# Kernel tuning notes

Hardware: AMD Instinct MI355X
Metric: run time of the kernel (lower is better)

The kernel has to match this reference:

```python
import jax, jax.numpy as jnp
import numpy as np

# Dims: C cells, L gene tokens, E embed, H mlp hidden, M factors, K topk
C, L, E, H, M, K = 16, 8192, 512, 256, 128, 30
TAU = 1.0        # gumbel-softmax temperature
SOFTNESS = 0.01  # soft-mask sharpness
TEMP = 1.0       # logits temperature
EPS = 1e-20


def setup_inputs() -> dict:
    key = jax.random.key(0)
    ks = jax.random.split(key, 7)
    x = jax.random.normal(ks[0], (C, L, E), dtype=jnp.float32)
    key_padding_mask = jax.random.randint(ks[1], (C, L), 0, 2) > 0  # True = valid
    uniform_noise = jax.random.uniform(ks[2], (C, L - 1, M), dtype=jnp.float32)
    W1 = jax.random.normal(ks[3], (E, H), dtype=jnp.float32) * (1.0 / np.sqrt(E))
    b1 = jnp.zeros((H,), dtype=jnp.float32)
    W2 = jax.random.normal(ks[4], (H, M), dtype=jnp.float32) * (1.0 / np.sqrt(H))
    b2 = jnp.zeros((M,), dtype=jnp.float32)
    return {"x": x, "key_padding_mask": key_padding_mask,
            "uniform_noise": uniform_noise,
            "W1": W1, "b1": b1, "W2": W2, "b2": b2}


def reference(x, key_padding_mask, uniform_noise, W1, b1, W2, b2):
    # default gene_subset: drop token 0, keep the rest  -> S = L-1
    xs = x[:, 1:, :]                          # (C, S, E)
    kpm = key_padding_mask[:, 1:]             # (C, S)

    # 2-layer MLP router (dropout p=0 -> identity)
    h = jax.nn.relu(jnp.einsum('cse,eh->csh', xs, W1) + b1)   # (C, S, H)
    logits = (jnp.einsum('csh,hm->csm', h, W2) + b2) / TEMP    # (C, S, M)

    # GumbelTopK, training path: gumbel-softmax then smooth top-k mask
    gumbel = -jnp.log(-jnp.log(uniform_noise + EPS) + EPS)
    perturbed = (logits + gumbel) / TAU
    probs = jax.nn.softmax(perturbed, axis=-1)                 # (C, S, M)
    topk_vals, _ = jax.lax.top_k(probs, K)                     # (C, S, K)
    threshold = topk_vals[..., -1:]                            # (C, S, 1)
    smooth_mask = jax.nn.sigmoid((probs - threshold) / SOFTNESS)
    out = probs * smooth_mask

    # faithful to the source: mask = ~key_padding_mask; probs *= mask
    out = out * (~kpm)[..., None].astype(out.dtype)
    return out, kpm
```

## Files before the change

### kernel.cpp

```cpp
#include <hip/hip_runtime.h>
#include <hip/hip_bf16.h>

#define CC 16
#define LL 8192
#define SS 8191
#define EE 512
#define HH 256
#define MM 128
#define TOPK 30
#define TOT (CC * SS)

typedef __attribute__((ext_vector_type(8))) short short8;
typedef __attribute__((ext_vector_type(4))) float f32x4;
typedef __attribute__((ext_vector_type(4))) unsigned int u32x4;

static __device__ __forceinline__ unsigned short f2bf(float f) {
    unsigned u = __builtin_bit_cast(unsigned, f);
    u += 0x7FFFu + ((u >> 16) & 1u);
    return (unsigned short)(u >> 16);
}

static __device__ __forceinline__ unsigned pk2(float lo, float hi) {
    __hip_bfloat162 t = __float22bfloat162_rn(float2{lo, hi});
    unsigned u;
    __builtin_memcpy(&u, &t, 4);
    return u;
}

static __device__ __forceinline__ short8 cvt8(const float4 a, const float4 b) {
    u32x4 uv;
    uv[0] = pk2(a.x, a.y);
    uv[1] = pk2(a.z, a.w);
    uv[2] = pk2(b.x, b.y);
    uv[3] = pk2(b.z, b.w);
    return __builtin_bit_cast(short8, uv);
}

template<int CTRL>
static __device__ __forceinline__ float dppf(float v) {
    return __builtin_bit_cast(float,
        __builtin_amdgcn_update_dpp(0, __builtin_bit_cast(int, v), CTRL, 0xF, 0xF, false));
}
template<int CTRL>
static __device__ __forceinline__ int dppi(int v) {
    return __builtin_amdgcn_update_dpp(0, v, CTRL, 0xF, 0xF, false);
}
static __device__ __forceinline__ float sum16f(float v) {
    v += dppf<0x121>(v); v += dppf<0x122>(v); v += dppf<0x124>(v); v += dppf<0x128>(v);
    return v;
}
static __device__ __forceinline__ float max16f(float v) {
    v = fmaxf(v, dppf<0x121>(v)); v = fmaxf(v, dppf<0x122>(v));
    v = fmaxf(v, dppf<0x124>(v)); v = fmaxf(v, dppf<0x128>(v));
    return v;
}
static __device__ __forceinline__ unsigned sum16u(unsigned v) {
    v += (unsigned)dppi<0x121>((int)v); v += (unsigned)dppi<0x122>((int)v);
    v += (unsigned)dppi<0x124>((int)v); v += (unsigned)dppi<0x128>((int)v);
    return v;
}

static __device__ __forceinline__ void bar_lgkm() {
    asm volatile("s_waitcnt lgkmcnt(0)" ::: "memory");
    __builtin_amdgcn_sched_barrier(0);
    __builtin_amdgcn_s_barrier();
    __builtin_amdgcn_sched_barrier(0);
}

__global__ void prep_weights(const float* __restrict__ W1, const float* __restrict__ W2,
                             unsigned short* __restrict__ W1T, unsigned short* __restrict__ W2T)
{
    const int b = blockIdx.x, tid = threadIdx.x;
    if (b < 64) {
        const int e0 = b * 8, h = tid;
        short8 sv;
#pragma unroll
        for (int j = 0; j < 8; ++j)
            sv[j] = (short)f2bf(W1[(size_t)(e0 + j) * HH + h]);
        *(short8*)(void*)(W1T + (size_t)h * EE + e0) = sv;
    } else {
        const int h0 = (b - 64) * 16;
        if (tid < MM) {
            const int m = tid;
            short8 s0v, s1v;
#pragma unroll
            for (int j = 0; j < 8; ++j) {
                s0v[j] = (short)f2bf(W2[(size_t)(h0 + j) * MM + m]);
                s1v[j] = (short)f2bf(W2[(size_t)(h0 + 8 + j) * MM + m]);
            }
            *(short8*)(void*)(W2T + (size_t)m * HH + h0) = s0v;
            *(short8*)(void*)(W2T + (size_t)m * HH + h0 + 8) = s1v;
        }
    }
}

__global__ __launch_bounds__(512, 4)
void gene_gemm_kernel(const float* __restrict__ x,
                      const unsigned short* __restrict__ W1T,
                      const float* __restrict__ b1,
                      const unsigned short* __restrict__ W2T,
                      float* __restrict__ logits)
{
    __shared__ __align__(16) unsigned char lds[65536];

    const int tid = threadIdx.x;
    const int c   = blockIdx.y;
    const int s0  = blockIdx.x * 128;

    const int w    = tid >> 6;
    const int lane = tid & 63;
    const int lr   = lane & 15;
    const int kq   = lane >> 4;
    const int wr   = w >> 2;
    const int wc   = w & 3;
    const int cw   = wc * 64;

    const int srow = tid >> 2;
    const int sk4  = tid & 3;
    const int rsc  = min(s0 + srow, SS - 1) - s0;
    const float* xrow = x + ((size_t)c * LL + s0 + 1 + rsc) * EE + sk4 * 16;
    const int swz = (srow & 7) << 4;
    unsigned char* wb = lds + srow * 128;

    float4 xr0, xr1, xr2, xr3;
#define LOADX(ck) do { const float* p_ = xrow + (ck) * 64;                   \
    xr0 = *(const float4*)p_;       xr1 = *(const float4*)(p_ + 4);          \
    xr2 = *(const float4*)(p_ + 8); xr3 = *(const float4*)(p_ + 12); } while (0)

    f32x4 acc[4][4];
#pragma unroll
    for (int r = 0; r < 4; ++r)
#pragma unroll
        for (int n = 0; n < 4; ++n) acc[r][n] = (f32x4)0.0f;

    LOADX(0);

#pragma unroll
    for (int ck = 0; ck < 8; ++ck) {
        const int bo = (ck & 1) << 14;
        *(short8*)(void*)(wb + bo + (((sk4 * 2 + 0) * 16) ^ swz)) = cvt8(xr0, xr1);
        *(short8*)(void*)(wb + bo + (((sk4 * 2 + 1) * 16) ^ swz)) = cvt8(xr2, xr3);
        if (ck < 7) LOADX(ck + 1);
        bar_lgkm();

#pragma unroll
        for (int ks = 0; ks < 2; ++ks) {
            short8 af[4];
#pragma unroll
            for (int r = 0; r < 4; ++r) {
                const int row = wr * 64 + r * 16 + lr;
                af[r] = *(const short8*)(const void*)
                    (lds + bo + row * 128 + (((ks * 4 + kq) * 16) ^ ((row & 7) << 4)));
            }
            short8 bf_[4];
#pragma unroll
            for (int n = 0; n < 4; ++n)
                bf_[n] = *(const short8*)(const void*)
                    (W1T + (size_t)(cw + n * 16 + lr) * EE + ck * 64 + ks * 32 + kq * 8);
#pragma unroll
            for (int r = 0; r < 4; ++r)
#pragma unroll
                for (int n = 0; n < 4; ++n)
                    acc[r][n] = __builtin_amdgcn_mfma_f32_16x16x32_bf16(af[r], bf_[n], acc[r][n], 0, 0, 0);
        }
        bar_lgkm();
    }

    float b1v[4];
#pragma unroll
    for (int n = 0; n < 4; ++n) b1v[n] = b1[cw + n * 16 + lr];

#pragma unroll
    for (int n = 0; n < 4; ++n) {
        const int colh = cw + n * 16 + lr;
#pragma unroll
        for (int r = 0; r < 4; ++r)
#pragma unroll
            for (int q = 0; q < 4; ++q) {
                const int row = wr * 64 + r * 16 + kq * 4 + q;
                *(unsigned short*)(lds + row * 512 + ((colh * 2) ^ ((row & 7) << 4))) =
                    f2bf(fmaxf(acc[r][n][q] + b1v[n], 0.0f));
            }
    }
    bar_lgkm();

    f32x4 acc2[4][2];
#pragma unroll
    for (int r = 0; r < 4; ++r)
#pragma unroll
        for (int n = 0; n < 2; ++n) acc2[r][n] = (f32x4)0.0f;

    const int cw2 = wc * 32;
#pragma unroll 4
    for (int ks = 0; ks < 8; ++ks) {
        short8 ah[4];
#pragma unroll
        for (int r = 0; r < 4; ++r) {
            const int row = wr * 64 + r * 16 + lr;
            ah[r] = *(const short8*)(const void*)
                (lds + row * 512 + ((ks * 64 + kq * 16) ^ ((row & 7) << 4)));
        }
        short8 bw[2];
#pragma unroll
        for (int n = 0; n < 2; ++n)
            bw[n] = *(const short8*)(const void*)
                (W2T + (size_t)(cw2 + n * 16 + lr) * HH + ks * 32 + kq * 8);
#pragma unroll
        for (int r = 0; r < 4; ++r)
#pragma unroll
            for (int n = 0; n < 2; ++n)
                acc2[r][n] = __builtin_amdgcn_mfma_f32_16x16x32_bf16(ah[r], bw[n], acc2[r][n], 0, 0, 0);
    }

#pragma unroll
    for (int r = 0; r < 4; ++r)
#pragma unroll
        for (int n = 0; n < 2; ++n)
#pragma unroll
            for (int q = 0; q < 4; ++q) {
                const int s = s0 + wr * 64 + r * 16 + kq * 4 + q;
                if (s < SS)
                    logits[((size_t)c * SS + s) * MM + cw2 + n * 16 + lr] = acc2[r][n][q];
            }
#undef LOADX
}

__global__ __launch_bounds__(256, 8)
void gene_epi_kernel(const float* __restrict__ noise,
                     const int*   __restrict__ mask,
                     const float* __restrict__ b2,
                     float* __restrict__ out,
                     float* __restrict__ outk)
{
    const int tid = threadIdx.x;
    const int tx  = tid & 15;
    const int ty  = tid >> 4;
    const long base = (long)blockIdx.x * 64;

    if (tid < 64) {
        const long gr = base + tid;
        if (gr < TOT) {
            const int cc2 = (int)(gr / SS);
            outk[gr] = (mask[gr + cc2 + 1] != 0) ? 1.0f : 0.0f;
        }
    }

    float b2v[8];
    {
        const float4 bb0 = *(const float4*)(b2 + tx * 8 + 0);
        const float4 bb1 = *(const float4*)(b2 + tx * 8 + 4);
        b2v[0]=bb0.x; b2v[1]=bb0.y; b2v[2]=bb0.z; b2v[3]=bb0.w;
        b2v[4]=bb1.x; b2v[5]=bb1.y; b2v[6]=bb1.z; b2v[7]=bb1.w;
    }

    float pr[4][8];
    float pmaxv[4];
    float mz[4];
    long  grv[4];

#pragma unroll
    for (int i = 0; i < 4; ++i) {
        const long gr  = base + ty * 4 + i;
        grv[i] = gr;
        const long grc = gr < TOT ? gr : (TOT - 1);
        const int  cc2 = (int)(grc / SS);
        mz[i] = (mask[grc + cc2 + 1] != 0) ? 0.0f : 1.0f;

        const float* lp = out   + grc * MM + tx * 8;
        const float* np = noise + grc * MM + tx * 8;
        const float4 l0 = *(const float4*)lp;
        const float4 l1 = *(const float4*)(lp + 4);
        const float4 u0 = *(const float4*)np;
        const float4 u1 = *(const float4*)(np + 4);
        const float lg[8] = {l0.x,l0.y,l0.z,l0.w,l1.x,l1.y,l1.z,l1.w};
        const float uu[8] = {u0.x,u0.y,u0.z,u0.w,u1.x,u1.y,u1.z,u1.w};
        float pm[8];
#pragma unroll
        for (int q = 0; q < 8; ++q) {
            const float g = -__logf(-__logf(uu[q] + 1e-20f) + 1e-20f);
            pm[q] = lg[q] + b2v[q] + g;
        }
        float mx = pm[0];
#pragma unroll
        for (int q = 1; q < 8; ++q) mx = fmaxf(mx, pm[q]);
        mx = max16f(mx);
        float se = 0.0f;
#pragma unroll
        for (int q = 0; q < 8; ++q) { pr[i][q] = __expf(pm[q] - mx); se += pr[i][q]; }
        se = sum16f(se);
        const float inv = 1.0f / se;
#pragma unroll
        for (int q = 0; q < 8; ++q) pr[i][q] *= inv;
        pmaxv[i] = inv;
    }

    float lo[4], hi[4];
#pragma unroll
    for (int i = 0; i < 4; ++i) { lo[i] = 0.0f; hi[i] = fminf(pmaxv[i], 1.0f / 30.0f); }
    for (int it = 0; it < 10; ++it) {
        float mid[4];
#pragma unroll
        for (int i = 0; i < 4; ++i) mid[i] = 0.5f * (lo[i] + hi[i]);
        unsigned cnt = 0;
#pragma unroll
        for (int q = 0; q < 8; ++q) {
            cnt += (pr[0][q] > mid[0]) ? 1u : 0u;
            cnt += (pr[1][q] > mid[1]) ? (1u << 8) : 0u;
            cnt += (pr[2][q] > mid[2]) ? (1u << 16) : 0u;
            cnt += (pr[3][q] > mid[3]) ? (1u << 24) : 0u;
        }
        cnt = sum16u(cnt);
#pragma unroll
        for (int i = 0; i < 4; ++i) {
            const bool ge = ((cnt >> (8 * i)) & 255u) >= TOPK;
            lo[i] = ge ? mid[i] : lo[i];
            hi[i] = ge ? hi[i] : mid[i];
        }
    }

#pragma unroll
    for (int i = 0; i < 4; ++i) {
        if (grv[i] < TOT) {
            float ov[8];
#pragma unroll
            for (int q = 0; q < 8; ++q) {
                const float sm = 1.0f / (1.0f + __expf((hi[i] - pr[i][q]) * 100.0f));
                ov[q] = pr[i][q] * sm * mz[i];
            }
            float* op = out + grv[i] * MM + tx * 8;
            float4 o0, o1;
            o0.x=ov[0]; o0.y=ov[1]; o0.z=ov[2]; o0.w=ov[3];
            o1.x=ov[4]; o1.y=ov[5]; o1.z=ov[6]; o1.w=ov[7];
            *(float4*)(op + 0) = o0;
            *(float4*)(op + 4) = o1;
        }
    }
}

extern "C" void kernel_launch(void* const* d_in, const int* in_sizes, int n_in,
                              void* d_out, int out_size, void* d_ws, size_t ws_size,
                              hipStream_t stream) {
    const float* x     = (const float*)d_in[0];
    const int*   mask  = (const int*)d_in[1];
    const float* noise = (const float*)d_in[2];
    const float* W1    = (const float*)d_in[3];
    const float* b1    = (const float*)d_in[4];
    const float* W2    = (const float*)d_in[5];
    const float* b2    = (const float*)d_in[6];
    float* out  = (float*)d_out;
    float* outk = out + (size_t)CC * SS * MM;

    unsigned short* W1T = (unsigned short*)d_ws;
    unsigned short* W2T = W1T + (size_t)HH * EE;

    prep_weights<<<dim3(80), dim3(256), 0, stream>>>(W1, W2, W1T, W2T);

    gene_gemm_kernel<<<dim3(64, CC), dim3(512), 0, stream>>>(x, W1T, b1, W2T, out);

    const int nblk = (TOT + 63) / 64;
    gene_epi_kernel<<<dim3(nblk), dim3(256), 0, stream>>>(noise, mask, b2, out, outk);
}
```

Before: 181.0 us.

## Make each wave own a private 16-row slice to remove block barriers in router GEMM

The fused MLP GEMM kernel now gives each wave its own 16-row slice of tokens with a private LDS region. Every wave computes all 256 hidden columns and all 128 logits for its rows, so all block-level barriers go away. Blocks shrink to 256 threads with 32KB LDS, and the grid doubles. In exchange, each wave now loads the full W1T and W2T fragments from global memory (L2 traffic goes up about 4x), and the A-fragment reuse across MFMAs drops to one row tile. Correctness within a wave relies on implicit wave-level ordering of LDS accesses without explicit waits.

Result: slower. 462.3 us (+155.3%).

```diff
diff --git a/kernel.cpp b/kernel.cpp
--- a/kernel.cpp
+++ b/kernel.cpp
@@ -60,13 +60,6 @@
     return v;
 }
 
-static __device__ __forceinline__ void bar_lgkm() {
-    asm volatile("s_waitcnt lgkmcnt(0)" ::: "memory");
-    __builtin_amdgcn_sched_barrier(0);
-    __builtin_amdgcn_s_barrier();
-    __builtin_amdgcn_sched_barrier(0);
-}
-
 __global__ void prep_weights(const float* __restrict__ W1, const float* __restrict__ W2,
                              unsigned short* __restrict__ W1T, unsigned short* __restrict__ W2T)
 {
@@ -94,134 +87,97 @@
     }
 }
 
-__global__ __launch_bounds__(512, 4)
+__global__ __launch_bounds__(256, 4)
 void gene_gemm_kernel(const float* __restrict__ x,
                       const unsigned short* __restrict__ W1T,
                       const float* __restrict__ b1,
                       const unsigned short* __restrict__ W2T,
                       float* __restrict__ logits)
 {
-    __shared__ __align__(16) unsigned char lds[65536];
-
-    const int tid = threadIdx.x;
-    const int c   = blockIdx.y;
-    const int s0  = blockIdx.x * 128;
-
+    __shared__ __align__(16) unsigned char lds[32768];
+
+    const int tid  = threadIdx.x;
+    const int c    = blockIdx.y;
     const int w    = tid >> 6;
     const int lane = tid & 63;
     const int lr   = lane & 15;
     const int kq   = lane >> 4;
-    const int wr   = w >> 2;
-    const int wc   = w & 3;
-    const int cw   = wc * 64;
-
-    const int srow = tid >> 2;
-    const int sk4  = tid & 3;
-    const int rsc  = min(s0 + srow, SS - 1) - s0;
-    const float* xrow = x + ((size_t)c * LL + s0 + 1 + rsc) * EE + sk4 * 16;
-    const int swz = (srow & 7) << 4;
-    unsigned char* wb = lds + srow * 128;
+    const int s0w  = blockIdx.x * 64 + w * 16;
+    unsigned char* slice = lds + w * 8192;
+
+    const int srow = lane >> 2;
+    const int sq   = lane & 3;
+    const int rsc  = min(s0w + srow, SS - 1);
+    const float* xrow = x + ((size_t)c * LL + 1 + rsc) * EE + sq * 16;
+    unsigned char* wbase = slice + srow * 128;
+    const int wswz = (srow & 7) << 4;
+    const int rswz = (lr & 7) << 4;
 
     float4 xr0, xr1, xr2, xr3;
 #define LOADX(ck) do { const float* p_ = xrow + (ck) * 64;                   \
     xr0 = *(const float4*)p_;       xr1 = *(const float4*)(p_ + 4);          \
     xr2 = *(const float4*)(p_ + 8); xr3 = *(const float4*)(p_ + 12); } while (0)
 
-    f32x4 acc[4][4];
-#pragma unroll
-    for (int r = 0; r < 4; ++r)
-#pragma unroll
-        for (int n = 0; n < 4; ++n) acc[r][n] = (f32x4)0.0f;
+    f32x4 acc[16];
+#pragma unroll
+    for (int n = 0; n < 16; ++n) acc[n] = (f32x4)0.0f;
 
     LOADX(0);
 
 #pragma unroll
     for (int ck = 0; ck < 8; ++ck) {
-        const int bo = (ck & 1) << 14;
-        *(short8*)(void*)(wb + bo + (((sk4 * 2 + 0) * 16) ^ swz)) = cvt8(xr0, xr1);
-        *(short8*)(void*)(wb + bo + (((sk4 * 2 + 1) * 16) ^ swz)) = cvt8(xr2, xr3);
+        const int bo = (ck & 1) << 11;
+        *(short8*)(void*)(wbase + bo + ((sq * 32 +  0) ^ wswz)) = cvt8(xr0, xr1);
+        *(short8*)(void*)(wbase + bo + ((sq * 32 + 16) ^ wswz)) = cvt8(xr2, xr3);
         if (ck < 7) LOADX(ck + 1);
-        bar_lgkm();
-
 #pragma unroll
         for (int ks = 0; ks < 2; ++ks) {
-            short8 af[4];
-#pragma unroll
-            for (int r = 0; r < 4; ++r) {
-                const int row = wr * 64 + r * 16 + lr;
-                af[r] = *(const short8*)(const void*)
-                    (lds + bo + row * 128 + (((ks * 4 + kq) * 16) ^ ((row & 7) << 4)));
+            const short8 af = *(const short8*)(const void*)
+                (slice + bo + lr * 128 + ((ks * 64 + kq * 16) ^ rswz));
+#pragma unroll
+            for (int n = 0; n < 16; ++n) {
+                const short8 bf_ = *(const short8*)(const void*)
+                    (W1T + (size_t)(n * 16 + lr) * EE + ck * 64 + ks * 32 + kq * 8);
+                acc[n] = __builtin_amdgcn_mfma_f32_16x16x32_bf16(af, bf_, acc[n], 0, 0, 0);
             }
-            short8 bf_[4];
-#pragma unroll
-            for (int n = 0; n < 4; ++n)
-                bf_[n] = *(const short8*)(const void*)
-                    (W1T + (size_t)(cw + n * 16 + lr) * EE + ck * 64 + ks * 32 + kq * 8);
-#pragma unroll
-            for (int r = 0; r < 4; ++r)
-#pragma unroll
-                for (int n = 0; n < 4; ++n)
-                    acc[r][n] = __builtin_amdgcn_mfma_f32_16x16x32_bf16(af[r], bf_[n], acc[r][n], 0, 0, 0);
-        }
-        bar_lgkm();
-    }
-
-    float b1v[4];
-#pragma unroll
-    for (int n = 0; n < 4; ++n) b1v[n] = b1[cw + n * 16 + lr];
-
-#pragma unroll
-    for (int n = 0; n < 4; ++n) {
-        const int colh = cw + n * 16 + lr;
-#pragma unroll
-        for (int r = 0; r < 4; ++r)
-#pragma unroll
-            for (int q = 0; q < 4; ++q) {
-                const int row = wr * 64 + r * 16 + kq * 4 + q;
-                *(unsigned short*)(lds + row * 512 + ((colh * 2) ^ ((row & 7) << 4))) =
-                    f2bf(fmaxf(acc[r][n][q] + b1v[n], 0.0f));
-            }
-    }
-    bar_lgkm();
-
-    f32x4 acc2[4][2];
-#pragma unroll
-    for (int r = 0; r < 4; ++r)
-#pragma unroll
-        for (int n = 0; n < 2; ++n) acc2[r][n] = (f32x4)0.0f;
-
-    const int cw2 = wc * 32;
-#pragma unroll 4
+        }
+    }
+
+#pragma unroll
+    for (int n = 0; n < 16; ++n) {
+        const float bb = b1[n * 16 + lr];
+#pragma unroll
+        for (int q = 0; q < 4; ++q) {
+            const int row = kq * 4 + q;
+            *(unsigned short*)(slice + row * 512 + (((n * 16 + lr) * 2) ^ ((row & 7) << 4))) =
+                f2bf(fmaxf(acc[n][q] + bb, 0.0f));
+        }
+    }
+
+    f32x4 acc2[8];
+#pragma unroll
+    for (int n = 0; n < 8; ++n) acc2[n] = (f32x4)0.0f;
+
+#pragma unroll
     for (int ks = 0; ks < 8; ++ks) {
-        short8 ah[4];
-#pragma unroll
-        for (int r = 0; r < 4; ++r) {
-            const int row = wr * 64 + r * 16 + lr;
-            ah[r] = *(const short8*)(const void*)
-                (lds + row * 512 + ((ks * 64 + kq * 16) ^ ((row & 7) << 4)));
-        }
-        short8 bw[2];
-#pragma unroll
-        for (int n = 0; n < 2; ++n)
-            bw[n] = *(const short8*)(const void*)
-                (W2T + (size_t)(cw2 + n * 16 + lr) * HH + ks * 32 + kq * 8);
-#pragma unroll
-        for (int r = 0; r < 4; ++r)
-#pragma unroll
-            for (int n = 0; n < 2; ++n)
-                acc2[r][n] = __builtin_amdgcn_mfma_f32_16x16x32_bf16(ah[r], bw[n], acc2[r][n], 0, 0, 0);
-    }
-
-#pragma unroll
-    for (int r = 0; r < 4; ++r)
-#pragma unroll
-        for (int n = 0; n < 2; ++n)
-#pragma unroll
-            for (int q = 0; q < 4; ++q) {
-                const int s = s0 + wr * 64 + r * 16 + kq * 4 + q;
-                if (s < SS)
-                    logits[((size_t)c * SS + s) * MM + cw2 + n * 16 + lr] = acc2[r][n][q];
-            }
+        const short8 ah = *(const short8*)(const void*)
+            (slice + lr * 512 + ((ks * 64 + kq * 16) ^ rswz));
+#pragma unroll
+        for (int n = 0; n < 8; ++n) {
+            const short8 bw = *(const short8*)(const void*)
+                (W2T + (size_t)(n * 16 + lr) * HH + ks * 32 + kq * 8);
+            acc2[n] = __builtin_amdgcn_mfma_f32_16x16x32_bf16(ah, bw, acc2[n], 0, 0, 0);
+        }
+    }
+
+#pragma unroll
+    for (int n = 0; n < 8; ++n)
+#pragma unroll
+        for (int q = 0; q < 4; ++q) {
+            const int s = s0w + kq * 4 + q;
+            if (s < SS)
+                logits[((size_t)c * SS + s) * MM + n * 16 + lr] = acc2[n][q];
+        }
 #undef LOADX
 }
 
@@ -355,7 +311,7 @@
 
     prep_weights<<<dim3(80), dim3(256), 0, stream>>>(W1, W2, W1T, W2T);
 
-    gene_gemm_kernel<<<dim3(64, CC), dim3(512), 0, stream>>>(x, W1T, b1, W2T, out);
+    gene_gemm_kernel<<<dim3(128, CC), dim3(256), 0, stream>>>(x, W1T, b1, W2T, out);
 
     const int nblk = (TOT + 63) / 64;
     gene_epi_kernel<<<dim3(nblk), dim3(256), 0, stream>>>(noise, mask, b2, out, outk);
```

## Split MLP into hidden-layer kernel and fused second-GEMM plus gumbel-topk epilogue

Applied to the files above, without the earlier changes.

The first kernel now computes only the ReLU hidden layer, using 64-row tiles and higher occupancy, and writes it as bf16 into the output buffer. A second kernel loads those hidden rows into LDS, runs the second GEMM with MFMA, and keeps the logits in LDS. It then applies the gumbel-softmax and top-k mask directly, so fp32 logits never round-trip through global memory. Loads and stores of x, noise, h and the output use nontemporal hints. The bf16 intermediate costs about as much memory traffic as the fp32 logits it replaces, and the smaller tiles make W1 fetches more redundant.

After: 295.7 us. 63.3% more time.

```diff
diff --git a/kernel.cpp b/kernel.cpp
--- a/kernel.cpp
+++ b/kernel.cpp
@@ -27,12 +27,12 @@
     return u;
 }
 
-static __device__ __forceinline__ short8 cvt8(const float4 a, const float4 b) {
+static __device__ __forceinline__ short8 cvt8(const f32x4 a, const f32x4 b) {
     u32x4 uv;
-    uv[0] = pk2(a.x, a.y);
-    uv[1] = pk2(a.z, a.w);
-    uv[2] = pk2(b.x, b.y);
-    uv[3] = pk2(b.z, b.w);
+    uv[0] = pk2(a[0], a[1]);
+    uv[1] = pk2(a[2], a[3]);
+    uv[2] = pk2(b[0], b[1]);
+    uv[3] = pk2(b[2], b[3]);
     return __builtin_bit_cast(short8, uv);
 }
 
@@ -94,18 +94,17 @@
     }
 }
 
-__global__ __launch_bounds__(512, 4)
-void gene_gemm_kernel(const float* __restrict__ x,
-                      const unsigned short* __restrict__ W1T,
-                      const float* __restrict__ b1,
-                      const unsigned short* __restrict__ W2T,
-                      float* __restrict__ logits)
+__global__ __launch_bounds__(512, 6)
+void gene_h_kernel(const float* __restrict__ x,
+                   const unsigned short* __restrict__ W1T,
+                   const float* __restrict__ b1,
+                   unsigned short* __restrict__ hb)
 {
-    __shared__ __align__(16) unsigned char lds[65536];
-
-    const int tid = threadIdx.x;
-    const int c   = blockIdx.y;
-    const int s0  = blockIdx.x * 128;
+    __shared__ __align__(16) unsigned char lds[16384];
+
+    const int tid  = threadIdx.x;
+    const int c    = blockIdx.y;
+    const int s0   = blockIdx.x * 64;
 
     const int w    = tid >> 6;
     const int lane = tid & 63;
@@ -115,21 +114,25 @@
     const int wc   = w & 3;
     const int cw   = wc * 64;
 
-    const int srow = tid >> 2;
-    const int sk4  = tid & 3;
-    const int rsc  = min(s0 + srow, SS - 1) - s0;
-    const float* xrow = x + ((size_t)c * LL + s0 + 1 + rsc) * EE + sk4 * 16;
-    const int swz = (srow & 7) << 4;
-    unsigned char* wb = lds + srow * 128;
-
-    float4 xr0, xr1, xr2, xr3;
-#define LOADX(ck) do { const float* p_ = xrow + (ck) * 64;                   \
-    xr0 = *(const float4*)p_;       xr1 = *(const float4*)(p_ + 4);          \
-    xr2 = *(const float4*)(p_ + 8); xr3 = *(const float4*)(p_ + 12); } while (0)
-
-    f32x4 acc[4][4];
-#pragma unroll
-    for (int r = 0; r < 4; ++r)
+    const int srow = tid >> 3;
+    const int sk   = tid & 7;
+    const int rsc  = min(s0 + srow, SS - 1);
+    const float* xrow = x + ((size_t)c * LL + 1 + rsc) * EE + sk * 8;
+    unsigned char* wbase = lds + srow * 128;
+    const int wswz = (srow & 7) << 4;
+
+    f32x4 xr0, xr1;
+#define LOADX(ck) do { const f32x4* p_ = (const f32x4*)(xrow + (ck) * 64);    \
+    xr0 = __builtin_nontemporal_load(p_);                                     \
+    xr1 = __builtin_nontemporal_load(p_ + 1); } while (0)
+
+    float b1v[4];
+#pragma unroll
+    for (int n = 0; n < 4; ++n) b1v[n] = b1[cw + n * 16 + lr];
+
+    f32x4 acc[2][4];
+#pragma unroll
+    for (int r = 0; r < 2; ++r)
 #pragma unroll
         for (int n = 0; n < 4; ++n) acc[r][n] = (f32x4)0.0f;
 
@@ -137,105 +140,69 @@
 
 #pragma unroll
     for (int ck = 0; ck < 8; ++ck) {
-        const int bo = (ck & 1) << 14;
-        *(short8*)(void*)(wb + bo + (((sk4 * 2 + 0) * 16) ^ swz)) = cvt8(xr0, xr1);
-        *(short8*)(void*)(wb + bo + (((sk4 * 2 + 1) * 16) ^ swz)) = cvt8(xr2, xr3);
+        const int bo = (ck & 1) << 13;
+        *(short8*)(void*)(wbase + bo + ((sk * 16) ^ wswz)) = cvt8(xr0, xr1);
         if (ck < 7) LOADX(ck + 1);
         bar_lgkm();
 
 #pragma unroll
         for (int ks = 0; ks < 2; ++ks) {
-            short8 af[4];
-#pragma unroll
-            for (int r = 0; r < 4; ++r) {
-                const int row = wr * 64 + r * 16 + lr;
+            short8 af[2];
+#pragma unroll
+            for (int r = 0; r < 2; ++r) {
+                const int row = wr * 32 + r * 16 + lr;
                 af[r] = *(const short8*)(const void*)
-                    (lds + bo + row * 128 + (((ks * 4 + kq) * 16) ^ ((row & 7) << 4)));
-            }
-            short8 bf_[4];
-#pragma unroll
-            for (int n = 0; n < 4; ++n)
-                bf_[n] = *(const short8*)(const void*)
+                    (lds + bo + row * 128 + ((ks * 64 + kq * 16) ^ ((row & 7) << 4)));
+            }
+#pragma unroll
+            for (int n = 0; n < 4; ++n) {
+                const short8 bf_ = *(const short8*)(const void*)
                     (W1T + (size_t)(cw + n * 16 + lr) * EE + ck * 64 + ks * 32 + kq * 8);
 #pragma unroll
-            for (int r = 0; r < 4; ++r)
-#pragma unroll
-                for (int n = 0; n < 4; ++n)
-                    acc[r][n] = __builtin_amdgcn_mfma_f32_16x16x32_bf16(af[r], bf_[n], acc[r][n], 0, 0, 0);
+                for (int r = 0; r < 2; ++r)
+                    acc[r][n] = __builtin_amdgcn_mfma_f32_16x16x32_bf16(af[r], bf_, acc[r][n], 0, 0, 0);
+            }
         }
         bar_lgkm();
     }
 
-    float b1v[4];
-#pragma unroll
-    for (int n = 0; n < 4; ++n) b1v[n] = b1[cw + n * 16 + lr];
-
 #pragma unroll
     for (int n = 0; n < 4; ++n) {
-        const int colh = cw + n * 16 + lr;
-#pragma unroll
-        for (int r = 0; r < 4; ++r)
+        const int col = cw + n * 16 + lr;
+#pragma unroll
+        for (int r = 0; r < 2; ++r)
 #pragma unroll
             for (int q = 0; q < 4; ++q) {
-                const int row = wr * 64 + r * 16 + kq * 4 + q;
-                *(unsigned short*)(lds + row * 512 + ((colh * 2) ^ ((row & 7) << 4))) =
-                    f2bf(fmaxf(acc[r][n][q] + b1v[n], 0.0f));
-            }
-    }
-    bar_lgkm();
-
-    f32x4 acc2[4][2];
-#pragma unroll
-    for (int r = 0; r < 4; ++r)
-#pragma unroll
-        for (int n = 0; n < 2; ++n) acc2[r][n] = (f32x4)0.0f;
-
-    const int cw2 = wc * 32;
-#pragma unroll 4
-    for (int ks = 0; ks < 8; ++ks) {
-        short8 ah[4];
-#pragma unroll
-        for (int r = 0; r < 4; ++r) {
-            const int row = wr * 64 + r * 16 + lr;
-            ah[r] = *(const short8*)(const void*)
-                (lds + row * 512 + ((ks * 64 + kq * 16) ^ ((row & 7) << 4)));
-        }
-        short8 bw[2];
-#pragma unroll
-        for (int n = 0; n < 2; ++n)
-            bw[n] = *(const short8*)(const void*)
-                (W2T + (size_t)(cw2 + n * 16 + lr) * HH + ks * 32 + kq * 8);
-#pragma unroll
-        for (int r = 0; r < 4; ++r)
-#pragma unroll
-            for (int n = 0; n < 2; ++n)
-                acc2[r][n] = __builtin_amdgcn_mfma_f32_16x16x32_bf16(ah[r], bw[n], acc2[r][n], 0, 0, 0);
-    }
-
-#pragma unroll
-    for (int r = 0; r < 4; ++r)
-#pragma unroll
-        for (int n = 0; n < 2; ++n)
-#pragma unroll
-            for (int q = 0; q < 4; ++q) {
-                const int s = s0 + wr * 64 + r * 16 + kq * 4 + q;
-                if (s < SS)
-                    logits[((size_t)c * SS + s) * MM + cw2 + n * 16 + lr] = acc2[r][n][q];
-            }
+                const int s = s0 + wr * 32 + r * 16 + kq * 4 + q;
+                if (s < SS) {
+                    const unsigned short hv = f2bf(fmaxf(acc[r][n][q] + b1v[n], 0.0f));
+                    __builtin_nontemporal_store(hv, hb + ((size_t)c * SS + s) * HH + col);
+                }
+            }
+    }
 #undef LOADX
 }
 
-__global__ __launch_bounds__(256, 8)
-void gene_epi_kernel(const float* __restrict__ noise,
+__global__ __launch_bounds__(256, 4)
+void gene_out_kernel(const unsigned short* __restrict__ hb,
+                     const float* __restrict__ noise,
                      const int*   __restrict__ mask,
+                     const unsigned short* __restrict__ W2T,
                      const float* __restrict__ b2,
                      float* __restrict__ out,
                      float* __restrict__ outk)
 {
-    const int tid = threadIdx.x;
-    const int tx  = tid & 15;
-    const int ty  = tid >> 4;
+    __shared__ __align__(16) unsigned char lds[33792];
+    float* sLf = (float*)lds;
+
+    const int tid  = threadIdx.x;
     const long base = (long)blockIdx.x * 64;
+    const int lane = tid & 63;
+    const int lr   = lane & 15;
+    const int kq   = lane >> 4;
+    const int wc   = tid >> 6;
+    const int tx   = tid & 15;
+    const int ty   = tid >> 4;
 
     if (tid < 64) {
         const long gr = base + tid;
@@ -244,6 +211,62 @@
             outk[gr] = (mask[gr + cc2 + 1] != 0) ? 1.0f : 0.0f;
         }
     }
+
+    {
+        const int row = tid >> 2;
+        const int skq = tid & 3;
+        const long grc = min(base + row, (long)TOT - 1);
+        const unsigned short* hrow = hb + grc * HH + skq * 64;
+        unsigned char* wb = lds + row * 512;
+        const int swz = (row & 7) << 4;
+#pragma unroll
+        for (int u = 0; u < 8; ++u) {
+            const short8 v = __builtin_nontemporal_load((const short8*)(const void*)(hrow + u * 8));
+            *(short8*)(void*)(wb + (((skq * 8 + u) * 16) ^ swz)) = v;
+        }
+    }
+    __syncthreads();
+
+    f32x4 acc2[4][2];
+#pragma unroll
+    for (int r = 0; r < 4; ++r)
+#pragma unroll
+        for (int n = 0; n < 2; ++n) acc2[r][n] = (f32x4)0.0f;
+
+    const int cw2 = wc * 32;
+#pragma unroll
+    for (int ks = 0; ks < 8; ++ks) {
+        short8 ah[4];
+#pragma unroll
+        for (int r = 0; r < 4; ++r) {
+            const int row = r * 16 + lr;
+            ah[r] = *(const short8*)(const void*)
+                (lds + row * 512 + ((ks * 64 + kq * 16) ^ ((row & 7) << 4)));
+        }
+        short8 bw[2];
+#pragma unroll
+        for (int n = 0; n < 2; ++n)
+            bw[n] = *(const short8*)(const void*)
+                (W2T + (size_t)(cw2 + n * 16 + lr) * HH + ks * 32 + kq * 8);
+#pragma unroll
+        for (int r = 0; r < 4; ++r)
+#pragma unroll
+            for (int n = 0; n < 2; ++n)
+                acc2[r][n] = __builtin_amdgcn_mfma_f32_16x16x32_bf16(ah[r], bw[n], acc2[r][n], 0, 0, 0);
+    }
+    __syncthreads();
+
+#pragma unroll
+    for (int r = 0; r < 4; ++r)
+#pragma unroll
+        for (int n = 0; n < 2; ++n)
+#pragma unroll
+            for (int q = 0; q < 4; ++q) {
+                const int row = r * 16 + kq * 4 + q;
+                const int col = cw2 + n * 16 + lr;
+                sLf[row * 132 + col] = acc2[r][n][q];
+            }
+    __syncthreads();
 
     float b2v[8];
     {
@@ -260,20 +283,20 @@
 
 #pragma unroll
     for (int i = 0; i < 4; ++i) {
-        const long gr  = base + ty * 4 + i;
+        const int row = ty * 4 + i;
+        const long gr = base + row;
         grv[i] = gr;
         const long grc = gr < TOT ? gr : (TOT - 1);
         const int  cc2 = (int)(grc / SS);
         mz[i] = (mask[grc + cc2 + 1] != 0) ? 0.0f : 1.0f;
 
-        const float* lp = out   + grc * MM + tx * 8;
-        const float* np = noise + grc * MM + tx * 8;
-        const float4 l0 = *(const float4*)lp;
-        const float4 l1 = *(const float4*)(lp + 4);
-        const float4 u0 = *(const float4*)np;
-        const float4 u1 = *(const float4*)(np + 4);
+        const f32x4* np = (const f32x4*)(noise + grc * MM + tx * 8);
+        const f32x4 u0 = __builtin_nontemporal_load(np);
+        const f32x4 u1 = __builtin_nontemporal_load(np + 1);
+        const float4 l0 = *(const float4*)&sLf[row * 132 + tx * 8];
+        const float4 l1 = *(const float4*)&sLf[row * 132 + tx * 8 + 4];
         const float lg[8] = {l0.x,l0.y,l0.z,l0.w,l1.x,l1.y,l1.z,l1.w};
-        const float uu[8] = {u0.x,u0.y,u0.z,u0.w,u1.x,u1.y,u1.z,u1.w};
+        const float uu[8] = {u0[0],u0[1],u0[2],u0[3],u1[0],u1[1],u1[2],u1[3]};
         float pm[8];
 #pragma unroll
         for (int q = 0; q < 8; ++q) {
@@ -327,12 +350,12 @@
                 const float sm = 1.0f / (1.0f + __expf((hi[i] - pr[i][q]) * 100.0f));
                 ov[q] = pr[i][q] * sm * mz[i];
             }
-            float* op = out + grv[i] * MM + tx * 8;
-            float4 o0, o1;
-            o0.x=ov[0]; o0.y=ov[1]; o0.z=ov[2]; o0.w=ov[3];
-            o1.x=ov[4]; o1.y=ov[5]; o1.z=ov[6]; o1.w=ov[7];
-            *(float4*)(op + 0) = o0;
-            *(float4*)(op + 4) = o1;
+            f32x4* op = (f32x4*)(out + grv[i] * MM + tx * 8);
+            f32x4 o0, o1;
+            o0[0]=ov[0]; o0[1]=ov[1]; o0[2]=ov[2]; o0[3]=ov[3];
+            o1[0]=ov[4]; o1[1]=ov[5]; o1[2]=ov[6]; o1[3]=ov[7];
+            __builtin_nontemporal_store(o0, op);
+            __builtin_nontemporal_store(o1, op + 1);
         }
     }
 }
@@ -352,11 +375,11 @@
 
     unsigned short* W1T = (unsigned short*)d_ws;
     unsigned short* W2T = W1T + (size_t)HH * EE;
+    unsigned short* hb  = (unsigned short*)d_out;
 
     prep_weights<<<dim3(80), dim3(256), 0, stream>>>(W1, W2, W1T, W2T);
 
-    gene_gemm_kernel<<<dim3(64, CC), dim3(512), 0, stream>>>(x, W1T, b1, W2T, out);
-
-    const int nblk = (TOT + 63) / 64;
-    gene_epi_kernel<<<dim3(nblk), dim3(256), 0, stream>>>(noise, mask, b2, out, outk);
-}
+    gene_h_kernel<<<dim3(128, CC), dim3(512), 0, stream>>>(x, W1T, b1, hb);
+
+    gene_out_kernel<<<dim3(2048), dim3(256), 0, stream>>>(hb, noise, mask, W2T, b2, out, outk);
+}
```
